# Optimization experiments

Hardware: AMD Instinct MI355X
Metric: run time of the kernel (lower is better)

Reference implementation:

```python
import jax, jax.numpy as jnp
import numpy as np

N_NODES = 50000
N_EDGES = 600000
IN_CH, HID_CH, OUT_CH = 128, 128, 64


def setup_inputs() -> dict:
    key = jax.random.key(0)
    ks = jax.random.split(key, 8)
    s = lambda fan_in: 1.0 / np.sqrt(fan_in)
    return {
        "x": jax.random.normal(ks[0], (N_NODES, IN_CH), dtype=jnp.float32),
        "edge_index": jax.random.randint(ks[1], (2, N_EDGES), 0, N_NODES, dtype=jnp.int32),
        "W1l": jax.random.normal(ks[2], (IN_CH, HID_CH), dtype=jnp.float32) * s(IN_CH),
        "W1r": jax.random.normal(ks[3], (IN_CH, HID_CH), dtype=jnp.float32) * s(IN_CH),
        "b1": jnp.zeros((HID_CH,), dtype=jnp.float32),
        "W2l": jax.random.normal(ks[4], (HID_CH, OUT_CH), dtype=jnp.float32) * s(HID_CH),
        "W2r": jax.random.normal(ks[5], (HID_CH, OUT_CH), dtype=jnp.float32) * s(HID_CH),
        "b2": jnp.zeros((OUT_CH,), dtype=jnp.float32),
    }


def _sage_conv(x, edge_index, Wl, Wr, b):
    """PyG SAGEConv (aggr='mean', root_weight=True): lin_l(mean_j x_j) + lin_r(x_i)."""
    src, dst = edge_index[0], edge_index[1]
    n = x.shape[0]
    # gather source features per edge, scatter-add into destination nodes
    agg = jax.ops.segment_sum(x[src], dst, num_segments=n)  # [N, F]
    deg = jax.ops.segment_sum(jnp.ones(src.shape, x.dtype), dst, num_segments=n)
    mean = agg / jnp.maximum(deg, 1.0)[:, None]
    return mean @ Wl + x @ Wr + b


def reference(x, edge_index, W1l, W1r, b1, W2l, W2r, b2):
    h = jax.nn.relu(_sage_conv(x, edge_index, W1l, W1r, b1))
    # dropout p=0.05 is identity in eval mode
    return _sage_conv(h, edge_index, W2l, W2r, b2)
```

## Files before the change

### kernel.cpp

```cpp
#include <hip/hip_runtime.h>
#include <hip/hip_bf16.h>

#define IN_CH 128
#define HID_CH 128
#define OUT_CH 64
#define SCAN_B 256

typedef __attribute__((ext_vector_type(8))) short bf16x8;
typedef __attribute__((ext_vector_type(4))) float f32x4;

__device__ __forceinline__ ushort f2bf(float f) {
    uint u = __float_as_uint(f);
    uint r = (u + 0x7fffu + ((u >> 16) & 1u)) >> 16;
    return (ushort)r;
}
__device__ __forceinline__ float bflo(uint u) { return __uint_as_float(u << 16); }
__device__ __forceinline__ float bfhi(uint u) { return __uint_as_float(u & 0xffff0000u); }


__global__ __launch_bounds__(256) void prep_count_kernel(
    const int* __restrict__ ei, int* __restrict__ deg,
    const float* __restrict__ x, ushort* __restrict__ xb,
    const float* __restrict__ W1l, const float* __restrict__ W1r,
    const float* __restrict__ W2l, const float* __restrict__ W2r,
    ushort* __restrict__ W1lT, ushort* __restrict__ W1rT,
    ushort* __restrict__ W2lT, ushort* __restrict__ W2rT,
    int n_edges, int nx, int cnt_blocks, int cvt_blocks) {
    int b = blockIdx.x, tid = threadIdx.x;
    if (b < cnt_blocks) {
        int e4 = b * 256 + tid;
        if (e4 * 4 < n_edges) {
            int4 d = *(const int4*)(ei + n_edges + e4 * 4);
            atomicAdd(&deg[d.x], 1);
            atomicAdd(&deg[d.y], 1);
            atomicAdd(&deg[d.z], 1);
            atomicAdd(&deg[d.w], 1);
        }
    } else if (b < cnt_blocks + cvt_blocks) {
        int i = (b - cnt_blocks) * 256 + tid;
        if (i * 8 < nx) {
            float4 v0 = *(const float4*)(x + i * 8);
            float4 v1 = *(const float4*)(x + i * 8 + 4);
            uint4 o;
            o.x = (uint)f2bf(v0.x) | ((uint)f2bf(v0.y) << 16);
            o.y = (uint)f2bf(v0.z) | ((uint)f2bf(v0.w) << 16);
            o.z = (uint)f2bf(v1.x) | ((uint)f2bf(v1.y) << 16);
            o.w = (uint)f2bf(v1.z) | ((uint)f2bf(v1.w) << 16);
            *(uint4*)(xb + i * 8) = o;
        }
    } else {
        int t = (b - cnt_blocks - cvt_blocks) * 256 + tid;
        if (t < 16384) {
            int nn = t >> 7, kk = t & 127;
            W1lT[t] = f2bf(W1l[kk * 128 + nn]);
        } else if (t < 32768) {
            int u = t - 16384;
            int nn = u >> 7, kk = u & 127;
            W1rT[u] = f2bf(W1r[kk * 128 + nn]);
        } else if (t < 40960) {
            int u = t - 32768;
            int nn = u >> 7, kk = u & 127;
            W2lT[u] = f2bf(W2l[kk * 64 + nn]);
        } else if (t < 49152) {
            int u = t - 40960;
            int nn = u >> 7, kk = u & 127;
            W2rT[u] = f2bf(W2r[kk * 64 + nn]);
        }
    }
}


__global__ __launch_bounds__(SCAN_B) void scan_partials_kernel(
    const int* __restrict__ deg, int* __restrict__ partials, int n) {
    __shared__ int ws[SCAN_B / 64];
    int i = blockIdx.x * SCAN_B + threadIdx.x;
    int v = (i < n) ? deg[i] : 0;
    for (int off = 32; off > 0; off >>= 1) v += __shfl_down(v, off, 64);
    int lane = threadIdx.x & 63, w = threadIdx.x >> 6;
    if (lane == 0) ws[w] = v;
    __syncthreads();
    if (threadIdx.x == 0) {
        int s = 0;
        for (int k = 0; k < SCAN_B / 64; ++k) s += ws[k];
        partials[blockIdx.x] = s;
    }
}

__global__ __launch_bounds__(256) void scan_bases_kernel(
    const int* __restrict__ partials, int* __restrict__ bases,
    int* __restrict__ offsets, int nblocks, int n) {
    __shared__ int sm[256];
    int t = threadIdx.x;
    int v = (t < nblocks) ? partials[t] : 0;
    sm[t] = v;
    __syncthreads();
    for (int off = 1; off < 256; off <<= 1) {
        int u = (t >= off) ? sm[t - off] : 0;
        __syncthreads();
        sm[t] += u;
        __syncthreads();
    }
    if (t < nblocks) bases[t] = sm[t] - v;
    if (t == 255) offsets[n] = sm[255];
}

__global__ __launch_bounds__(SCAN_B) void scan_final_kernel(
    const int* __restrict__ deg, const int* __restrict__ bases,
    int* __restrict__ offsets, int* __restrict__ cursor, int n) {
    __shared__ int sm[SCAN_B];
    int t = threadIdx.x;
    int i = blockIdx.x * SCAN_B + t;
    int v = (i < n) ? deg[i] : 0;
    sm[t] = v;
    __syncthreads();
    for (int off = 1; off < SCAN_B; off <<= 1) {
        int u = (t >= off) ? sm[t - off] : 0;
        __syncthreads();
        sm[t] += u;
        __syncthreads();
    }
    if (i < n) {
        int o = bases[blockIdx.x] + sm[t] - v;
        offsets[i] = o;
        cursor[i]  = o;
    }
}

__global__ __launch_bounds__(256) void fill_kernel(
    const int* __restrict__ ei, int* __restrict__ cursor,
    int* __restrict__ edge_src, int n_edges) {
    int e4 = blockIdx.x * 256 + threadIdx.x;
    if (e4 * 4 >= n_edges) return;
    int4 s = *(const int4*)(ei + e4 * 4);
    int4 d = *(const int4*)(ei + n_edges + e4 * 4);
    edge_src[atomicAdd(&cursor[d.x], 1)] = s.x;
    edge_src[atomicAdd(&cursor[d.y], 1)] = s.y;
    edge_src[atomicAdd(&cursor[d.z], 1)] = s.z;
    edge_src[atomicAdd(&cursor[d.w], 1)] = s.w;
}


__global__ __launch_bounds__(256) void gather_mean_bf16_kernel(
    const ushort* __restrict__ feat, const int* __restrict__ offsets,
    const int* __restrict__ edge_src, ushort* __restrict__ mean, int n_nodes) {
    int wid  = (blockIdx.x * blockDim.x + threadIdx.x) >> 6;
    int lane = threadIdx.x & 63;
    if (wid >= n_nodes) return;
    int beg = offsets[wid];
    int end = offsets[wid + 1];
    int q = lane >> 4;
    int c = lane & 15;
    float s0 = 0, s1 = 0, s2 = 0, s3 = 0, s4 = 0, s5 = 0, s6 = 0, s7 = 0;

    int e = beg;
    for (; e + 8 <= end; e += 8) {
        int r0 = edge_src[e + q];
        int r1 = edge_src[e + 4 + q];
        uint4 A = *(const uint4*)(feat + (size_t)r0 * 128 + c * 8);
        uint4 B = *(const uint4*)(feat + (size_t)r1 * 128 + c * 8);
        s0 += bflo(A.x) + bflo(B.x);  s1 += bfhi(A.x) + bfhi(B.x);
        s2 += bflo(A.y) + bflo(B.y);  s3 += bfhi(A.y) + bfhi(B.y);
        s4 += bflo(A.z) + bflo(B.z);  s5 += bfhi(A.z) + bfhi(B.z);
        s6 += bflo(A.w) + bflo(B.w);  s7 += bfhi(A.w) + bfhi(B.w);
    }
    int rem = end - e;
    if (rem > 0) {
        int i0 = min(e + q, end - 1);
        int i1 = min(e + 4 + q, end - 1);
        int r0 = edge_src[i0];
        int r1 = edge_src[i1];
        uint4 A = *(const uint4*)(feat + (size_t)r0 * 128 + c * 8);
        uint4 B = *(const uint4*)(feat + (size_t)r1 * 128 + c * 8);
        if (q < rem) {
            s0 += bflo(A.x);  s1 += bfhi(A.x);
            s2 += bflo(A.y);  s3 += bfhi(A.y);
            s4 += bflo(A.z);  s5 += bfhi(A.z);
            s6 += bflo(A.w);  s7 += bfhi(A.w);
        }
        if (4 + q < rem) {
            s0 += bflo(B.x);  s1 += bfhi(B.x);
            s2 += bflo(B.y);  s3 += bfhi(B.y);
            s4 += bflo(B.z);  s5 += bfhi(B.z);
            s6 += bflo(B.w);  s7 += bfhi(B.w);
        }
    }

#pragma unroll
    for (int m = 16; m < 64; m <<= 1) {
        s0 += __shfl_xor(s0, m, 64);
        s1 += __shfl_xor(s1, m, 64);
        s2 += __shfl_xor(s2, m, 64);
        s3 += __shfl_xor(s3, m, 64);
        s4 += __shfl_xor(s4, m, 64);
        s5 += __shfl_xor(s5, m, 64);
        s6 += __shfl_xor(s6, m, 64);
        s7 += __shfl_xor(s7, m, 64);
    }

    if (q == 0) {
        float inv = 1.0f / fmaxf((float)(end - beg), 1.0f);
        uint4 o;
        o.x = (uint)f2bf(s0 * inv) | ((uint)f2bf(s1 * inv) << 16);
        o.y = (uint)f2bf(s2 * inv) | ((uint)f2bf(s3 * inv) << 16);
        o.z = (uint)f2bf(s4 * inv) | ((uint)f2bf(s5 * inv) << 16);
        o.w = (uint)f2bf(s6 * inv) | ((uint)f2bf(s7 * inv) << 16);
        *(uint4*)(mean + (size_t)wid * 128 + c * 8) = o;
    }
}


__global__ __launch_bounds__(256) void l1_mfma_kernel(
    const ushort* __restrict__ mean, const ushort* __restrict__ xb,
    const ushort* __restrict__ WlT, const ushort* __restrict__ WrT,
    const float* __restrict__ b, ushort* __restrict__ h, int n_nodes) {
    int wave = threadIdx.x >> 6, lane = threadIdx.x & 63;
    int m0 = (blockIdx.x * 4 + wave) * 32;
    int r  = lane & 15;
    int ko = (lane >> 4) * 8;

    int gc0 = min(m0 + r,      n_nodes - 1);
    int gc1 = min(m0 + 16 + r, n_nodes - 1);

    f32x4 acc[8][2] = {};
#pragma unroll
    for (int kk = 0; kk < 4; ++kk) {
        int kb = kk * 32 + ko;
        bf16x8 aM0 = *(const bf16x8*)(mean + (size_t)gc0 * 128 + kb);
        bf16x8 aM1 = *(const bf16x8*)(mean + (size_t)gc1 * 128 + kb);
        bf16x8 aX0 = *(const bf16x8*)(xb   + (size_t)gc0 * 128 + kb);
        bf16x8 aX1 = *(const bf16x8*)(xb   + (size_t)gc1 * 128 + kb);
#pragma unroll
        for (int j = 0; j < 8; ++j) {
            bf16x8 bL = *(const bf16x8*)(WlT + (size_t)(j * 16 + r) * 128 + kb);
            bf16x8 bR = *(const bf16x8*)(WrT + (size_t)(j * 16 + r) * 128 + kb);
            acc[j][0] = __builtin_amdgcn_mfma_f32_16x16x32_bf16(aM0, bL, acc[j][0], 0, 0, 0);
            acc[j][0] = __builtin_amdgcn_mfma_f32_16x16x32_bf16(aX0, bR, acc[j][0], 0, 0, 0);
            acc[j][1] = __builtin_amdgcn_mfma_f32_16x16x32_bf16(aM1, bL, acc[j][1], 0, 0, 0);
            acc[j][1] = __builtin_amdgcn_mfma_f32_16x16x32_bf16(aX1, bR, acc[j][1], 0, 0, 0);
        }
    }

#pragma unroll
    for (int j = 0; j < 8; ++j) {
        float bv = b[j * 16 + r];
#pragma unroll
        for (int s = 0; s < 2; ++s) {
            int rowbase = m0 + s * 16 + (lane >> 4) * 4;
#pragma unroll
            for (int q = 0; q < 4; ++q) {
                int g = rowbase + q;
                if (g < n_nodes)
                    h[(size_t)g * 128 + j * 16 + r] =
                        f2bf(fmaxf(acc[j][s][q] + bv, 0.f));
            }
        }
    }
}


__global__ __launch_bounds__(256) void l2_mfma_kernel(
    const ushort* __restrict__ mean, const ushort* __restrict__ hb,
    const ushort* __restrict__ WlT, const ushort* __restrict__ WrT,
    const float* __restrict__ b, float* __restrict__ out, int n_nodes) {
    int wave = threadIdx.x >> 6, lane = threadIdx.x & 63;
    int m0 = (blockIdx.x * 4 + wave) * 32;
    int r  = lane & 15;
    int ko = (lane >> 4) * 8;

    int gc0 = min(m0 + r,      n_nodes - 1);
    int gc1 = min(m0 + 16 + r, n_nodes - 1);

    f32x4 acc[4][2] = {};
#pragma unroll
    for (int kk = 0; kk < 4; ++kk) {
        int kb = kk * 32 + ko;
        bf16x8 aM0 = *(const bf16x8*)(mean + (size_t)gc0 * 128 + kb);
        bf16x8 aM1 = *(const bf16x8*)(mean + (size_t)gc1 * 128 + kb);
        bf16x8 aH0 = *(const bf16x8*)(hb   + (size_t)gc0 * 128 + kb);
        bf16x8 aH1 = *(const bf16x8*)(hb   + (size_t)gc1 * 128 + kb);
#pragma unroll
        for (int j = 0; j < 4; ++j) {
            bf16x8 bL = *(const bf16x8*)(WlT + (size_t)(j * 16 + r) * 128 + kb);
            bf16x8 bR = *(const bf16x8*)(WrT + (size_t)(j * 16 + r) * 128 + kb);
            acc[j][0] = __builtin_amdgcn_mfma_f32_16x16x32_bf16(aM0, bL, acc[j][0], 0, 0, 0);
            acc[j][0] = __builtin_amdgcn_mfma_f32_16x16x32_bf16(aH0, bR, acc[j][0], 0, 0, 0);
            acc[j][1] = __builtin_amdgcn_mfma_f32_16x16x32_bf16(aM1, bL, acc[j][1], 0, 0, 0);
            acc[j][1] = __builtin_amdgcn_mfma_f32_16x16x32_bf16(aH1, bR, acc[j][1], 0, 0, 0);
        }
    }

#pragma unroll
    for (int j = 0; j < 4; ++j) {
        float bv = b[j * 16 + r];
#pragma unroll
        for (int s = 0; s < 2; ++s) {
            int rowbase = m0 + s * 16 + (lane >> 4) * 4;
#pragma unroll
            for (int q = 0; q < 4; ++q) {
                int g = rowbase + q;
                if (g < n_nodes)
                    out[(size_t)g * 64 + j * 16 + r] = acc[j][s][q] + bv;
            }
        }
    }
}


extern "C" void kernel_launch(void* const* d_in, const int* in_sizes, int n_in,
                              void* d_out, int out_size, void* d_ws, size_t ws_size,
                              hipStream_t stream) {
    const float* x   = (const float*)d_in[0];
    const int*   ei  = (const int*)d_in[1];
    const float* W1l = (const float*)d_in[2];
    const float* W1r = (const float*)d_in[3];
    const float* b1  = (const float*)d_in[4];
    const float* W2l = (const float*)d_in[5];
    const float* W2r = (const float*)d_in[6];
    const float* b2  = (const float*)d_in[7];
    float* out = (float*)d_out;

    int n_nodes = in_sizes[0] / IN_CH;
    int n_edges = in_sizes[1] / 2;
    int nsb = (n_nodes + SCAN_B - 1) / SCAN_B;

    char* ws = (char*)d_ws;
    int* deg      = (int*)ws;
    int* offsets  = deg + n_nodes;
    int* cursor   = offsets + n_nodes + 1;
    int* partials = cursor + n_nodes;
    int* bases    = partials + nsb;
    int* edge_src = bases + nsb;
    size_t off = ((size_t)(3 * n_nodes + 1 + 2 * nsb + n_edges)) * sizeof(int);
    off = (off + 255) & ~(size_t)255;
    ushort* xb    = (ushort*)(ws + off);
    ushort* meanb = xb    + (size_t)n_nodes * 128;
    ushort* hb    = meanb + (size_t)n_nodes * 128;
    ushort* W1lT  = hb    + (size_t)n_nodes * 128;
    ushort* W1rT  = W1lT + 128 * 128;
    ushort* W2lT  = W1rT + 128 * 128;
    ushort* W2rT  = W2lT + 64 * 128;

    hipMemsetAsync(deg, 0, n_nodes * sizeof(int), stream);

    const int TB = 256;
    int nx = n_nodes * IN_CH;
    int cnt_blocks = (n_edges / 4 + TB - 1) / TB;
    int cvt_blocks = (nx / 8 + TB - 1) / TB;
    int tr_blocks  = (49152 + TB - 1) / TB;

    prep_count_kernel<<<cnt_blocks + cvt_blocks + tr_blocks, TB, 0, stream>>>(
        ei, deg, x, xb, W1l, W1r, W2l, W2r, W1lT, W1rT, W2lT, W2rT,
        n_edges, nx, cnt_blocks, cvt_blocks);
    scan_partials_kernel<<<nsb, SCAN_B, 0, stream>>>(deg, partials, n_nodes);
    scan_bases_kernel<<<1, 256, 0, stream>>>(partials, bases, offsets, nsb, n_nodes);
    scan_final_kernel<<<nsb, SCAN_B, 0, stream>>>(deg, bases, offsets, cursor, n_nodes);
    fill_kernel<<<cnt_blocks, TB, 0, stream>>>(ei, cursor, edge_src, n_edges);

    int gblocks = (n_nodes * 64 + TB - 1) / TB;
    int mblocks = (n_nodes + 127) / 128;

    gather_mean_bf16_kernel<<<gblocks, TB, 0, stream>>>(xb, offsets, edge_src, meanb, n_nodes);
    l1_mfma_kernel<<<mblocks, 256, 0, stream>>>(meanb, xb, W1lT, W1rT, b1, hb, n_nodes);

    gather_mean_bf16_kernel<<<gblocks, TB, 0, stream>>>(hb, offsets, edge_src, meanb, n_nodes);
    l2_mfma_kernel<<<mblocks, 256, 0, stream>>>(meanb, hb, W2lT, W2rT, b2, out, n_nodes);
}
```

Before: 248.0 us.

## Fuse all stages into one persistent kernel with software grid barriers

Replaces the memset and nine kernel launches with a single persistent mega-kernel. The grid is sized from occupancy times CU count, and the stages (convert, degree count, scan, CSR fill, two gather/GEMM layers) are separated by atomic-counter grid barriers. The goal is to remove launch overhead and inter-kernel gaps. In exchange, each stage now runs as a grid-stride loop on fewer threads, and the barriers add spin costs. Correctness relies on all blocks being co-resident, since the launch is not cooperative. The gather tail is also simplified to use conditional loads.

New measurement: 751.2 us. 3.03x slower.

```diff
diff --git a/kernel.cpp b/kernel.cpp
--- a/kernel.cpp
+++ b/kernel.cpp
@@ -1,9 +1,5 @@
 #include <hip/hip_runtime.h>
-#include <hip/hip_bf16.h>
-
-#define IN_CH 128
-#define HID_CH 128
-#define OUT_CH 64
+
 #define SCAN_B 256
 
 typedef __attribute__((ext_vector_type(8))) short bf16x8;
@@ -17,135 +13,31 @@
 __device__ __forceinline__ float bflo(uint u) { return __uint_as_float(u << 16); }
 __device__ __forceinline__ float bfhi(uint u) { return __uint_as_float(u & 0xffff0000u); }
 
-
-__global__ __launch_bounds__(256) void prep_count_kernel(
-    const int* __restrict__ ei, int* __restrict__ deg,
-    const float* __restrict__ x, ushort* __restrict__ xb,
-    const float* __restrict__ W1l, const float* __restrict__ W1r,
-    const float* __restrict__ W2l, const float* __restrict__ W2r,
-    ushort* __restrict__ W1lT, ushort* __restrict__ W1rT,
-    ushort* __restrict__ W2lT, ushort* __restrict__ W2rT,
-    int n_edges, int nx, int cnt_blocks, int cvt_blocks) {
-    int b = blockIdx.x, tid = threadIdx.x;
-    if (b < cnt_blocks) {
-        int e4 = b * 256 + tid;
-        if (e4 * 4 < n_edges) {
-            int4 d = *(const int4*)(ei + n_edges + e4 * 4);
-            atomicAdd(&deg[d.x], 1);
-            atomicAdd(&deg[d.y], 1);
-            atomicAdd(&deg[d.z], 1);
-            atomicAdd(&deg[d.w], 1);
-        }
-    } else if (b < cnt_blocks + cvt_blocks) {
-        int i = (b - cnt_blocks) * 256 + tid;
-        if (i * 8 < nx) {
-            float4 v0 = *(const float4*)(x + i * 8);
-            float4 v1 = *(const float4*)(x + i * 8 + 4);
-            uint4 o;
-            o.x = (uint)f2bf(v0.x) | ((uint)f2bf(v0.y) << 16);
-            o.y = (uint)f2bf(v0.z) | ((uint)f2bf(v0.w) << 16);
-            o.z = (uint)f2bf(v1.x) | ((uint)f2bf(v1.y) << 16);
-            o.w = (uint)f2bf(v1.z) | ((uint)f2bf(v1.w) << 16);
-            *(uint4*)(xb + i * 8) = o;
-        }
-    } else {
-        int t = (b - cnt_blocks - cvt_blocks) * 256 + tid;
-        if (t < 16384) {
-            int nn = t >> 7, kk = t & 127;
-            W1lT[t] = f2bf(W1l[kk * 128 + nn]);
-        } else if (t < 32768) {
-            int u = t - 16384;
-            int nn = u >> 7, kk = u & 127;
-            W1rT[u] = f2bf(W1r[kk * 128 + nn]);
-        } else if (t < 40960) {
-            int u = t - 32768;
-            int nn = u >> 7, kk = u & 127;
-            W2lT[u] = f2bf(W2l[kk * 64 + nn]);
-        } else if (t < 49152) {
-            int u = t - 40960;
-            int nn = u >> 7, kk = u & 127;
-            W2rT[u] = f2bf(W2r[kk * 64 + nn]);
-        }
-    }
-}
-
-
-__global__ __launch_bounds__(SCAN_B) void scan_partials_kernel(
-    const int* __restrict__ deg, int* __restrict__ partials, int n) {
-    __shared__ int ws[SCAN_B / 64];
-    int i = blockIdx.x * SCAN_B + threadIdx.x;
-    int v = (i < n) ? deg[i] : 0;
-    for (int off = 32; off > 0; off >>= 1) v += __shfl_down(v, off, 64);
-    int lane = threadIdx.x & 63, w = threadIdx.x >> 6;
-    if (lane == 0) ws[w] = v;
+__device__ int g_bar_cnt = 0;
+__device__ int g_bar_gen = 0;
+
+__device__ __forceinline__ void grid_barrier() {
     __syncthreads();
     if (threadIdx.x == 0) {
-        int s = 0;
-        for (int k = 0; k < SCAN_B / 64; ++k) s += ws[k];
-        partials[blockIdx.x] = s;
-    }
-}
-
-__global__ __launch_bounds__(256) void scan_bases_kernel(
-    const int* __restrict__ partials, int* __restrict__ bases,
-    int* __restrict__ offsets, int nblocks, int n) {
-    __shared__ int sm[256];
-    int t = threadIdx.x;
-    int v = (t < nblocks) ? partials[t] : 0;
-    sm[t] = v;
+        __threadfence();
+        int g = __hip_atomic_load(&g_bar_gen, __ATOMIC_RELAXED, __HIP_MEMORY_SCOPE_AGENT);
+        int a = __hip_atomic_fetch_add(&g_bar_cnt, 1, __ATOMIC_ACQ_REL, __HIP_MEMORY_SCOPE_AGENT);
+        if (a == (int)gridDim.x - 1) {
+            __hip_atomic_store(&g_bar_cnt, 0, __ATOMIC_RELAXED, __HIP_MEMORY_SCOPE_AGENT);
+            __hip_atomic_fetch_add(&g_bar_gen, 1, __ATOMIC_RELEASE, __HIP_MEMORY_SCOPE_AGENT);
+        } else {
+            while (__hip_atomic_load(&g_bar_gen, __ATOMIC_ACQUIRE, __HIP_MEMORY_SCOPE_AGENT) == g)
+                __builtin_amdgcn_s_sleep(2);
+        }
+        __threadfence();
+    }
     __syncthreads();
-    for (int off = 1; off < 256; off <<= 1) {
-        int u = (t >= off) ? sm[t - off] : 0;
-        __syncthreads();
-        sm[t] += u;
-        __syncthreads();
-    }
-    if (t < nblocks) bases[t] = sm[t] - v;
-    if (t == 255) offsets[n] = sm[255];
-}
-
-__global__ __launch_bounds__(SCAN_B) void scan_final_kernel(
-    const int* __restrict__ deg, const int* __restrict__ bases,
-    int* __restrict__ offsets, int* __restrict__ cursor, int n) {
-    __shared__ int sm[SCAN_B];
-    int t = threadIdx.x;
-    int i = blockIdx.x * SCAN_B + t;
-    int v = (i < n) ? deg[i] : 0;
-    sm[t] = v;
-    __syncthreads();
-    for (int off = 1; off < SCAN_B; off <<= 1) {
-        int u = (t >= off) ? sm[t - off] : 0;
-        __syncthreads();
-        sm[t] += u;
-        __syncthreads();
-    }
-    if (i < n) {
-        int o = bases[blockIdx.x] + sm[t] - v;
-        offsets[i] = o;
-        cursor[i]  = o;
-    }
-}
-
-__global__ __launch_bounds__(256) void fill_kernel(
-    const int* __restrict__ ei, int* __restrict__ cursor,
-    int* __restrict__ edge_src, int n_edges) {
-    int e4 = blockIdx.x * 256 + threadIdx.x;
-    if (e4 * 4 >= n_edges) return;
-    int4 s = *(const int4*)(ei + e4 * 4);
-    int4 d = *(const int4*)(ei + n_edges + e4 * 4);
-    edge_src[atomicAdd(&cursor[d.x], 1)] = s.x;
-    edge_src[atomicAdd(&cursor[d.y], 1)] = s.y;
-    edge_src[atomicAdd(&cursor[d.z], 1)] = s.z;
-    edge_src[atomicAdd(&cursor[d.w], 1)] = s.w;
-}
-
-
-__global__ __launch_bounds__(256) void gather_mean_bf16_kernel(
+}
+
+__device__ __forceinline__ void gather_node(
     const ushort* __restrict__ feat, const int* __restrict__ offsets,
-    const int* __restrict__ edge_src, ushort* __restrict__ mean, int n_nodes) {
-    int wid  = (blockIdx.x * blockDim.x + threadIdx.x) >> 6;
-    int lane = threadIdx.x & 63;
-    if (wid >= n_nodes) return;
+    const int* __restrict__ edge_src, ushort* __restrict__ mean,
+    int wid, int lane) {
     int beg = offsets[wid];
     int end = offsets[wid + 1];
     int q = lane >> 4;
@@ -163,26 +55,21 @@
         s4 += bflo(A.z) + bflo(B.z);  s5 += bfhi(A.z) + bfhi(B.z);
         s6 += bflo(A.w) + bflo(B.w);  s7 += bfhi(A.w) + bfhi(B.w);
     }
-    int rem = end - e;
-    if (rem > 0) {
-        int i0 = min(e + q, end - 1);
-        int i1 = min(e + 4 + q, end - 1);
-        int r0 = edge_src[i0];
-        int r1 = edge_src[i1];
+    if (e + q < end) {
+        int r0 = edge_src[e + q];
         uint4 A = *(const uint4*)(feat + (size_t)r0 * 128 + c * 8);
+        s0 += bflo(A.x);  s1 += bfhi(A.x);
+        s2 += bflo(A.y);  s3 += bfhi(A.y);
+        s4 += bflo(A.z);  s5 += bfhi(A.z);
+        s6 += bflo(A.w);  s7 += bfhi(A.w);
+    }
+    if (e + 4 + q < end) {
+        int r1 = edge_src[e + 4 + q];
         uint4 B = *(const uint4*)(feat + (size_t)r1 * 128 + c * 8);
-        if (q < rem) {
-            s0 += bflo(A.x);  s1 += bfhi(A.x);
-            s2 += bflo(A.y);  s3 += bfhi(A.y);
-            s4 += bflo(A.z);  s5 += bfhi(A.z);
-            s6 += bflo(A.w);  s7 += bfhi(A.w);
-        }
-        if (4 + q < rem) {
-            s0 += bflo(B.x);  s1 += bfhi(B.x);
-            s2 += bflo(B.y);  s3 += bfhi(B.y);
-            s4 += bflo(B.z);  s5 += bfhi(B.z);
-            s6 += bflo(B.w);  s7 += bfhi(B.w);
-        }
+        s0 += bflo(B.x);  s1 += bfhi(B.x);
+        s2 += bflo(B.y);  s3 += bfhi(B.y);
+        s4 += bflo(B.z);  s5 += bfhi(B.z);
+        s6 += bflo(B.w);  s7 += bfhi(B.w);
     }
 
 #pragma unroll
@@ -208,16 +95,13 @@
     }
 }
 
-
-__global__ __launch_bounds__(256) void l1_mfma_kernel(
+__device__ __forceinline__ void l1_tile(
     const ushort* __restrict__ mean, const ushort* __restrict__ xb,
     const ushort* __restrict__ WlT, const ushort* __restrict__ WrT,
-    const float* __restrict__ b, ushort* __restrict__ h, int n_nodes) {
-    int wave = threadIdx.x >> 6, lane = threadIdx.x & 63;
-    int m0 = (blockIdx.x * 4 + wave) * 32;
+    const float* __restrict__ b, ushort* __restrict__ h,
+    int m0, int lane, int n_nodes) {
     int r  = lane & 15;
     int ko = (lane >> 4) * 8;
-
     int gc0 = min(m0 + r,      n_nodes - 1);
     int gc1 = min(m0 + 16 + r, n_nodes - 1);
 
@@ -239,7 +123,6 @@
             acc[j][1] = __builtin_amdgcn_mfma_f32_16x16x32_bf16(aX1, bR, acc[j][1], 0, 0, 0);
         }
     }
-
 #pragma unroll
     for (int j = 0; j < 8; ++j) {
         float bv = b[j * 16 + r];
@@ -247,26 +130,23 @@
         for (int s = 0; s < 2; ++s) {
             int rowbase = m0 + s * 16 + (lane >> 4) * 4;
 #pragma unroll
-            for (int q = 0; q < 4; ++q) {
-                int g = rowbase + q;
+            for (int q2 = 0; q2 < 4; ++q2) {
+                int g = rowbase + q2;
                 if (g < n_nodes)
                     h[(size_t)g * 128 + j * 16 + r] =
-                        f2bf(fmaxf(acc[j][s][q] + bv, 0.f));
+                        f2bf(fmaxf(acc[j][s][q2] + bv, 0.f));
             }
         }
     }
 }
 
-
-__global__ __launch_bounds__(256) void l2_mfma_kernel(
+__device__ __forceinline__ void l2_tile(
     const ushort* __restrict__ mean, const ushort* __restrict__ hb,
     const ushort* __restrict__ WlT, const ushort* __restrict__ WrT,
-    const float* __restrict__ b, float* __restrict__ out, int n_nodes) {
-    int wave = threadIdx.x >> 6, lane = threadIdx.x & 63;
-    int m0 = (blockIdx.x * 4 + wave) * 32;
+    const float* __restrict__ b, float* __restrict__ out,
+    int m0, int lane, int n_nodes) {
     int r  = lane & 15;
     int ko = (lane >> 4) * 8;
-
     int gc0 = min(m0 + r,      n_nodes - 1);
     int gc1 = min(m0 + 16 + r, n_nodes - 1);
 
@@ -288,7 +168,6 @@
             acc[j][1] = __builtin_amdgcn_mfma_f32_16x16x32_bf16(aH1, bR, acc[j][1], 0, 0, 0);
         }
     }
-
 #pragma unroll
     for (int j = 0; j < 4; ++j) {
         float bv = b[j * 16 + r];
@@ -296,72 +175,181 @@
         for (int s = 0; s < 2; ++s) {
             int rowbase = m0 + s * 16 + (lane >> 4) * 4;
 #pragma unroll
-            for (int q = 0; q < 4; ++q) {
-                int g = rowbase + q;
+            for (int q2 = 0; q2 < 4; ++q2) {
+                int g = rowbase + q2;
                 if (g < n_nodes)
-                    out[(size_t)g * 64 + j * 16 + r] = acc[j][s][q] + bv;
+                    out[(size_t)g * 64 + j * 16 + r] = acc[j][s][q2] + bv;
             }
         }
     }
+}
+
+struct Params {
+    const int* ei; const float* x;
+    const float* W1l; const float* W1r; const float* b1;
+    const float* W2l; const float* W2r; const float* b2;
+    int* deg; int* offsets; int* cursor; int* partials; int* edge_src;
+    ushort* xb; ushort* meanb; ushort* hb;
+    ushort* W1lT; ushort* W1rT; ushort* W2lT; ushort* W2rT;
+    float* out;
+    int n_nodes, n_edges, nsb;
+};
+
+__global__ __launch_bounds__(256, 2) void mega_kernel(Params p) {
+    int tid  = threadIdx.x;
+    int gt   = blockIdx.x * 256 + tid;
+    int nthr = gridDim.x * 256;
+    int lane = tid & 63;
+    int wave = tid >> 6;
+    __shared__ int sA[SCAN_B];
+    __shared__ int sB[SCAN_B];
+
+    for (int i = gt; i < p.n_nodes; i += nthr) p.deg[i] = 0;
+    int nx8 = p.n_nodes * 128 / 8;
+    for (int i = gt; i < nx8; i += nthr) {
+        float4 v0 = *(const float4*)(p.x + (size_t)i * 8);
+        float4 v1 = *(const float4*)(p.x + (size_t)i * 8 + 4);
+        uint4 o;
+        o.x = (uint)f2bf(v0.x) | ((uint)f2bf(v0.y) << 16);
+        o.y = (uint)f2bf(v0.z) | ((uint)f2bf(v0.w) << 16);
+        o.z = (uint)f2bf(v1.x) | ((uint)f2bf(v1.y) << 16);
+        o.w = (uint)f2bf(v1.z) | ((uint)f2bf(v1.w) << 16);
+        *(uint4*)(p.xb + (size_t)i * 8) = o;
+    }
+    for (int t = gt; t < 49152; t += nthr) {
+        if (t < 16384)       { int nn = t >> 7, kk = t & 127;            p.W1lT[t] = f2bf(p.W1l[kk * 128 + nn]); }
+        else if (t < 32768)  { int u = t - 16384; int nn = u >> 7, kk = u & 127; p.W1rT[u] = f2bf(p.W1r[kk * 128 + nn]); }
+        else if (t < 40960)  { int u = t - 32768; int nn = u >> 7, kk = u & 127; p.W2lT[u] = f2bf(p.W2l[kk * 64 + nn]); }
+        else                 { int u = t - 40960; int nn = u >> 7, kk = u & 127; p.W2rT[u] = f2bf(p.W2r[kk * 64 + nn]); }
+    }
+    grid_barrier();
+
+    int ne4 = p.n_edges >> 2;
+    for (int e4 = gt; e4 < ne4; e4 += nthr) {
+        int4 d = *(const int4*)(p.ei + p.n_edges + (size_t)e4 * 4);
+        atomicAdd(&p.deg[d.x], 1); atomicAdd(&p.deg[d.y], 1);
+        atomicAdd(&p.deg[d.z], 1); atomicAdd(&p.deg[d.w], 1);
+    }
+    for (int e = ne4 * 4 + gt; e < p.n_edges; e += nthr)
+        atomicAdd(&p.deg[p.ei[p.n_edges + e]], 1);
+    grid_barrier();
+
+    for (int ch = blockIdx.x; ch < p.nsb; ch += gridDim.x) {
+        int i = ch * SCAN_B + tid;
+        int v = (i < p.n_nodes) ? p.deg[i] : 0;
+        for (int m = 32; m > 0; m >>= 1) v += __shfl_down(v, m, 64);
+        if (lane == 0) sA[wave] = v;
+        __syncthreads();
+        if (tid == 0) p.partials[ch] = sA[0] + sA[1] + sA[2] + sA[3];
+        __syncthreads();
+    }
+    grid_barrier();
+
+    for (int ch = blockIdx.x; ch < p.nsb; ch += gridDim.x) {
+        sA[tid] = (tid < p.nsb) ? p.partials[tid] : 0;
+        __syncthreads();
+        for (int m = 1; m < SCAN_B; m <<= 1) {
+            int u = (tid >= m) ? sA[tid - m] : 0;
+            __syncthreads();
+            sA[tid] += u;
+            __syncthreads();
+        }
+        int base  = (ch > 0) ? sA[ch - 1] : 0;
+        int total = sA[p.nsb - 1];
+        int i = ch * SCAN_B + tid;
+        int v = (i < p.n_nodes) ? p.deg[i] : 0;
+        sB[tid] = v;
+        __syncthreads();
+        for (int m = 1; m < SCAN_B; m <<= 1) {
+            int u = (tid >= m) ? sB[tid - m] : 0;
+            __syncthreads();
+            sB[tid] += u;
+            __syncthreads();
+        }
+        if (i < p.n_nodes) {
+            int o = base + sB[tid] - v;
+            p.offsets[i] = o;
+            p.cursor[i]  = o;
+        }
+        if (ch == p.nsb - 1 && tid == 0) p.offsets[p.n_nodes] = total;
+        __syncthreads();
+    }
+    grid_barrier();
+
+    for (int e4 = gt; e4 < ne4; e4 += nthr) {
+        int4 s = *(const int4*)(p.ei + (size_t)e4 * 4);
+        int4 d = *(const int4*)(p.ei + p.n_edges + (size_t)e4 * 4);
+        p.edge_src[atomicAdd(&p.cursor[d.x], 1)] = s.x;
+        p.edge_src[atomicAdd(&p.cursor[d.y], 1)] = s.y;
+        p.edge_src[atomicAdd(&p.cursor[d.z], 1)] = s.z;
+        p.edge_src[atomicAdd(&p.cursor[d.w], 1)] = s.w;
+    }
+    for (int e = ne4 * 4 + gt; e < p.n_edges; e += nthr) {
+        int s = p.ei[e], d = p.ei[p.n_edges + e];
+        p.edge_src[atomicAdd(&p.cursor[d], 1)] = s;
+    }
+    grid_barrier();
+
+    int gw = blockIdx.x * 4 + wave, nw = gridDim.x * 4;
+    for (int wid = gw; wid < p.n_nodes; wid += nw)
+        gather_node(p.xb, p.offsets, p.edge_src, p.meanb, wid, lane);
+    grid_barrier();
+
+    for (int t0 = blockIdx.x * 128; t0 < p.n_nodes; t0 += gridDim.x * 128)
+        l1_tile(p.meanb, p.xb, p.W1lT, p.W1rT, p.b1, p.hb, t0 + wave * 32, lane, p.n_nodes);
+    grid_barrier();
+
+    for (int wid = gw; wid < p.n_nodes; wid += nw)
+        gather_node(p.hb, p.offsets, p.edge_src, p.meanb, wid, lane);
+    grid_barrier();
+
+    for (int t0 = blockIdx.x * 128; t0 < p.n_nodes; t0 += gridDim.x * 128)
+        l2_tile(p.meanb, p.hb, p.W2lT, p.W2rT, p.b2, p.out, t0 + wave * 32, lane, p.n_nodes);
 }
 
 
 extern "C" void kernel_launch(void* const* d_in, const int* in_sizes, int n_in,
                               void* d_out, int out_size, void* d_ws, size_t ws_size,
                               hipStream_t stream) {
-    const float* x   = (const float*)d_in[0];
-    const int*   ei  = (const int*)d_in[1];
-    const float* W1l = (const float*)d_in[2];
-    const float* W1r = (const float*)d_in[3];
-    const float* b1  = (const float*)d_in[4];
-    const float* W2l = (const float*)d_in[5];
-    const float* W2r = (const float*)d_in[6];
-    const float* b2  = (const float*)d_in[7];
-    float* out = (float*)d_out;
-
-    int n_nodes = in_sizes[0] / IN_CH;
-    int n_edges = in_sizes[1] / 2;
-    int nsb = (n_nodes + SCAN_B - 1) / SCAN_B;
-
-    char* ws = (char*)d_ws;
-    int* deg      = (int*)ws;
-    int* offsets  = deg + n_nodes;
-    int* cursor   = offsets + n_nodes + 1;
-    int* partials = cursor + n_nodes;
-    int* bases    = partials + nsb;
-    int* edge_src = bases + nsb;
-    size_t off = ((size_t)(3 * n_nodes + 1 + 2 * nsb + n_edges)) * sizeof(int);
+    Params p;
+    p.x   = (const float*)d_in[0];
+    p.ei  = (const int*)d_in[1];
+    p.W1l = (const float*)d_in[2];
+    p.W1r = (const float*)d_in[3];
+    p.b1  = (const float*)d_in[4];
+    p.W2l = (const float*)d_in[5];
+    p.W2r = (const float*)d_in[6];
+    p.b2  = (const float*)d_in[7];
+    p.out = (float*)d_out;
+
+    p.n_nodes = in_sizes[0] / 128;
+    p.n_edges = in_sizes[1] / 2;
+    p.nsb = (p.n_nodes + SCAN_B - 1) / SCAN_B;
+
+    char* ws   = (char*)d_ws;
+    p.deg      = (int*)ws;
+    p.offsets  = p.deg + p.n_nodes;
+    p.cursor   = p.offsets + p.n_nodes + 1;
+    p.partials = p.cursor + p.n_nodes;
+    p.edge_src = p.partials + p.nsb;
+    size_t off = ((size_t)(3 * p.n_nodes + 1 + p.nsb + p.n_edges)) * sizeof(int);
     off = (off + 255) & ~(size_t)255;
-    ushort* xb    = (ushort*)(ws + off);
-    ushort* meanb = xb    + (size_t)n_nodes * 128;
-    ushort* hb    = meanb + (size_t)n_nodes * 128;
-    ushort* W1lT  = hb    + (size_t)n_nodes * 128;
-    ushort* W1rT  = W1lT + 128 * 128;
-    ushort* W2lT  = W1rT + 128 * 128;
-    ushort* W2rT  = W2lT + 64 * 128;
-
-    hipMemsetAsync(deg, 0, n_nodes * sizeof(int), stream);
-
-    const int TB = 256;
-    int nx = n_nodes * IN_CH;
-    int cnt_blocks = (n_edges / 4 + TB - 1) / TB;
-    int cvt_blocks = (nx / 8 + TB - 1) / TB;
-    int tr_blocks  = (49152 + TB - 1) / TB;
-
-    prep_count_kernel<<<cnt_blocks + cvt_blocks + tr_blocks, TB, 0, stream>>>(
-        ei, deg, x, xb, W1l, W1r, W2l, W2r, W1lT, W1rT, W2lT, W2rT,
-        n_edges, nx, cnt_blocks, cvt_blocks);
-    scan_partials_kernel<<<nsb, SCAN_B, 0, stream>>>(deg, partials, n_nodes);
-    scan_bases_kernel<<<1, 256, 0, stream>>>(partials, bases, offsets, nsb, n_nodes);
-    scan_final_kernel<<<nsb, SCAN_B, 0, stream>>>(deg, bases, offsets, cursor, n_nodes);
-    fill_kernel<<<cnt_blocks, TB, 0, stream>>>(ei, cursor, edge_src, n_edges);
-
-    int gblocks = (n_nodes * 64 + TB - 1) / TB;
-    int mblocks = (n_nodes + 127) / 128;
-
-    gather_mean_bf16_kernel<<<gblocks, TB, 0, stream>>>(xb, offsets, edge_src, meanb, n_nodes);
-    l1_mfma_kernel<<<mblocks, 256, 0, stream>>>(meanb, xb, W1lT, W1rT, b1, hb, n_nodes);
-
-    gather_mean_bf16_kernel<<<gblocks, TB, 0, stream>>>(hb, offsets, edge_src, meanb, n_nodes);
-    l2_mfma_kernel<<<mblocks, 256, 0, stream>>>(meanb, hb, W2lT, W2rT, b2, out, n_nodes);
-}
+    p.xb    = (ushort*)(ws + off);
+    p.meanb = p.xb    + (size_t)p.n_nodes * 128;
+    p.hb    = p.meanb + (size_t)p.n_nodes * 128;
+    p.W1lT  = p.hb    + (size_t)p.n_nodes * 128;
+    p.W1rT  = p.W1lT + 128 * 128;
+    p.W2lT  = p.W1rT + 128 * 128;
+    p.W2rT  = p.W2lT + 64 * 128;
+
+    int maxActive = 0;
+    (void)hipOccupancyMaxActiveBlocksPerMultiprocessor(&maxActive, mega_kernel, 256, 0);
+    if (maxActive < 1) maxActive = 1;
+    if (maxActive > 8) maxActive = 8;
+    int nCU = 0;
+    (void)hipDeviceGetAttribute(&nCU, hipDeviceAttributeMultiprocessorCount, 0);
+    if (nCU <= 0) nCU = 256;
+    int grid = maxActive * nCU;
+
+    hipLaunchKernelGGL(mega_kernel, dim3(grid), dim3(256), 0, stream, p);
+}
```

## Project layer-2 features before aggregation and merge scan base kernel into final scan

Applied to the files above, without the earlier changes.

Layer 2 now computes h@W2l first into a 64-wide bf16 buffer, then gathers and means those 64-wide rows, and finally adds h@W2r plus bias in a separate MFMA kernel. Because the mean is linear, this halves the bytes moved by the second gather. It adds one extra kernel launch and an extra round trip through a 64-wide intermediate, and rounds the projected values to bf16 before aggregation. The scan is also simplified: each final-scan block redoes the scan of block partials itself, which removes the single-block bases kernel. The gather tail now guards each load with a bounds check instead of clamping indices.

New measurement: 250.2 us. About the same (+0.9%).

```diff
diff --git a/kernel.cpp b/kernel.cpp
--- a/kernel.cpp
+++ b/kernel.cpp
@@ -2,8 +2,6 @@
 #include <hip/hip_bf16.h>
 
 #define IN_CH 128
-#define HID_CH 128
-#define OUT_CH 64
 #define SCAN_B 256
 
 typedef __attribute__((ext_vector_type(8))) short bf16x8;
@@ -86,44 +84,38 @@
     }
 }
 
-__global__ __launch_bounds__(256) void scan_bases_kernel(
-    const int* __restrict__ partials, int* __restrict__ bases,
-    int* __restrict__ offsets, int nblocks, int n) {
-    __shared__ int sm[256];
+__global__ __launch_bounds__(SCAN_B) void scan_final_kernel(
+    const int* __restrict__ deg, const int* __restrict__ partials,
+    int* __restrict__ offsets, int* __restrict__ cursor, int n, int nsb) {
+    __shared__ int sA[SCAN_B];
+    __shared__ int sB[SCAN_B];
     int t = threadIdx.x;
-    int v = (t < nblocks) ? partials[t] : 0;
-    sm[t] = v;
+    sA[t] = (t < nsb) ? partials[t] : 0;
     __syncthreads();
-    for (int off = 1; off < 256; off <<= 1) {
-        int u = (t >= off) ? sm[t - off] : 0;
+    for (int m = 1; m < SCAN_B; m <<= 1) {
+        int u = (t >= m) ? sA[t - m] : 0;
         __syncthreads();
-        sm[t] += u;
+        sA[t] += u;
         __syncthreads();
     }
-    if (t < nblocks) bases[t] = sm[t] - v;
-    if (t == 255) offsets[n] = sm[255];
-}
-
-__global__ __launch_bounds__(SCAN_B) void scan_final_kernel(
-    const int* __restrict__ deg, const int* __restrict__ bases,
-    int* __restrict__ offsets, int* __restrict__ cursor, int n) {
-    __shared__ int sm[SCAN_B];
-    int t = threadIdx.x;
+    int base  = (blockIdx.x > 0) ? sA[blockIdx.x - 1] : 0;
+    int total = sA[nsb - 1];
     int i = blockIdx.x * SCAN_B + t;
     int v = (i < n) ? deg[i] : 0;
-    sm[t] = v;
+    sB[t] = v;
     __syncthreads();
-    for (int off = 1; off < SCAN_B; off <<= 1) {
-        int u = (t >= off) ? sm[t - off] : 0;
+    for (int m = 1; m < SCAN_B; m <<= 1) {
+        int u = (t >= m) ? sB[t - m] : 0;
         __syncthreads();
-        sm[t] += u;
+        sB[t] += u;
         __syncthreads();
     }
     if (i < n) {
-        int o = bases[blockIdx.x] + sm[t] - v;
+        int o = base + sB[t] - v;
         offsets[i] = o;
         cursor[i]  = o;
     }
+    if (blockIdx.x == 0 && t == 0) offsets[n] = total;
 }
 
 __global__ __launch_bounds__(256) void fill_kernel(
@@ -140,7 +132,7 @@
 }
 
 
-__global__ __launch_bounds__(256) void gather_mean_bf16_kernel(
+__global__ __launch_bounds__(256) void gather_mean128_kernel(
     const ushort* __restrict__ feat, const int* __restrict__ offsets,
     const int* __restrict__ edge_src, ushort* __restrict__ mean, int n_nodes) {
     int wid  = (blockIdx.x * blockDim.x + threadIdx.x) >> 6;
@@ -163,26 +155,21 @@
         s4 += bflo(A.z) + bflo(B.z);  s5 += bfhi(A.z) + bfhi(B.z);
         s6 += bflo(A.w) + bflo(B.w);  s7 += bfhi(A.w) + bfhi(B.w);
     }
-    int rem = end - e;
-    if (rem > 0) {
-        int i0 = min(e + q, end - 1);
-        int i1 = min(e + 4 + q, end - 1);
-        int r0 = edge_src[i0];
-        int r1 = edge_src[i1];
+    if (e + q < end) {
+        int r0 = edge_src[e + q];
         uint4 A = *(const uint4*)(feat + (size_t)r0 * 128 + c * 8);
+        s0 += bflo(A.x);  s1 += bfhi(A.x);
+        s2 += bflo(A.y);  s3 += bfhi(A.y);
+        s4 += bflo(A.z);  s5 += bfhi(A.z);
+        s6 += bflo(A.w);  s7 += bfhi(A.w);
+    }
+    if (e + 4 + q < end) {
+        int r1 = edge_src[e + 4 + q];
         uint4 B = *(const uint4*)(feat + (size_t)r1 * 128 + c * 8);
-        if (q < rem) {
-            s0 += bflo(A.x);  s1 += bfhi(A.x);
-            s2 += bflo(A.y);  s3 += bfhi(A.y);
-            s4 += bflo(A.z);  s5 += bfhi(A.z);
-            s6 += bflo(A.w);  s7 += bfhi(A.w);
-        }
-        if (4 + q < rem) {
-            s0 += bflo(B.x);  s1 += bfhi(B.x);
-            s2 += bflo(B.y);  s3 += bfhi(B.y);
-            s4 += bflo(B.z);  s5 += bfhi(B.z);
-            s6 += bflo(B.w);  s7 += bfhi(B.w);
-        }
+        s0 += bflo(B.x);  s1 += bfhi(B.x);
+        s2 += bflo(B.y);  s3 += bfhi(B.y);
+        s4 += bflo(B.z);  s5 += bfhi(B.z);
+        s6 += bflo(B.w);  s7 += bfhi(B.w);
     }
 
 #pragma unroll
@@ -209,6 +196,70 @@
 }
 
 
+__global__ __launch_bounds__(256) void gather_mean64_kernel(
+    const ushort* __restrict__ feat, const int* __restrict__ offsets,
+    const int* __restrict__ edge_src, ushort* __restrict__ mean, int n_nodes) {
+    int wid  = (blockIdx.x * blockDim.x + threadIdx.x) >> 6;
+    int lane = threadIdx.x & 63;
+    if (wid >= n_nodes) return;
+    int beg = offsets[wid];
+    int end = offsets[wid + 1];
+    int q = lane >> 3;
+    int c = lane & 7;
+    float s0 = 0, s1 = 0, s2 = 0, s3 = 0, s4 = 0, s5 = 0, s6 = 0, s7 = 0;
+
+    int e = beg;
+    for (; e + 16 <= end; e += 16) {
+        int r0 = edge_src[e + q];
+        int r1 = edge_src[e + 8 + q];
+        uint4 A = *(const uint4*)(feat + (size_t)r0 * 64 + c * 8);
+        uint4 B = *(const uint4*)(feat + (size_t)r1 * 64 + c * 8);
+        s0 += bflo(A.x) + bflo(B.x);  s1 += bfhi(A.x) + bfhi(B.x);
+        s2 += bflo(A.y) + bflo(B.y);  s3 += bfhi(A.y) + bfhi(B.y);
+        s4 += bflo(A.z) + bflo(B.z);  s5 += bfhi(A.z) + bfhi(B.z);
+        s6 += bflo(A.w) + bflo(B.w);  s7 += bfhi(A.w) + bfhi(B.w);
+    }
+    if (e + q < end) {
+        int r0 = edge_src[e + q];
+        uint4 A = *(const uint4*)(feat + (size_t)r0 * 64 + c * 8);
+        s0 += bflo(A.x);  s1 += bfhi(A.x);
+        s2 += bflo(A.y);  s3 += bfhi(A.y);
+        s4 += bflo(A.z);  s5 += bfhi(A.z);
+        s6 += bflo(A.w);  s7 += bfhi(A.w);
+    }
+    if (e + 8 + q < end) {
+        int r1 = edge_src[e + 8 + q];
+        uint4 B = *(const uint4*)(feat + (size_t)r1 * 64 + c * 8);
+        s0 += bflo(B.x);  s1 += bfhi(B.x);
+        s2 += bflo(B.y);  s3 += bfhi(B.y);
+        s4 += bflo(B.z);  s5 += bfhi(B.z);
+        s6 += bflo(B.w);  s7 += bfhi(B.w);
+    }
+
+#pragma unroll
+    for (int m = 8; m < 64; m <<= 1) {
+        s0 += __shfl_xor(s0, m, 64);
+        s1 += __shfl_xor(s1, m, 64);
+        s2 += __shfl_xor(s2, m, 64);
+        s3 += __shfl_xor(s3, m, 64);
+        s4 += __shfl_xor(s4, m, 64);
+        s5 += __shfl_xor(s5, m, 64);
+        s6 += __shfl_xor(s6, m, 64);
+        s7 += __shfl_xor(s7, m, 64);
+    }
+
+    if (q == 0) {
+        float inv = 1.0f / fmaxf((float)(end - beg), 1.0f);
+        uint4 o;
+        o.x = (uint)f2bf(s0 * inv) | ((uint)f2bf(s1 * inv) << 16);
+        o.y = (uint)f2bf(s2 * inv) | ((uint)f2bf(s3 * inv) << 16);
+        o.z = (uint)f2bf(s4 * inv) | ((uint)f2bf(s5 * inv) << 16);
+        o.w = (uint)f2bf(s6 * inv) | ((uint)f2bf(s7 * inv) << 16);
+        *(uint4*)(mean + (size_t)wid * 64 + c * 8) = o;
+    }
+}
+
+
 __global__ __launch_bounds__(256) void l1_mfma_kernel(
     const ushort* __restrict__ mean, const ushort* __restrict__ xb,
     const ushort* __restrict__ WlT, const ushort* __restrict__ WrT,
@@ -258,10 +309,9 @@
 }
 
 
-__global__ __launch_bounds__(256) void l2_mfma_kernel(
-    const ushort* __restrict__ mean, const ushort* __restrict__ hb,
-    const ushort* __restrict__ WlT, const ushort* __restrict__ WrT,
-    const float* __restrict__ b, float* __restrict__ out, int n_nodes) {
+__global__ __launch_bounds__(256) void l2p_mfma_kernel(
+    const ushort* __restrict__ hb, const ushort* __restrict__ WlT,
+    ushort* __restrict__ hp, int n_nodes) {
     int wave = threadIdx.x >> 6, lane = threadIdx.x & 63;
     int m0 = (blockIdx.x * 4 + wave) * 32;
     int r  = lane & 15;
@@ -274,24 +324,17 @@
 #pragma unroll
     for (int kk = 0; kk < 4; ++kk) {
         int kb = kk * 32 + ko;
-        bf16x8 aM0 = *(const bf16x8*)(mean + (size_t)gc0 * 128 + kb);
-        bf16x8 aM1 = *(const bf16x8*)(mean + (size_t)gc1 * 128 + kb);
-        bf16x8 aH0 = *(const bf16x8*)(hb   + (size_t)gc0 * 128 + kb);
-        bf16x8 aH1 = *(const bf16x8*)(hb   + (size_t)gc1 * 128 + kb);
+        bf16x8 aH0 = *(const bf16x8*)(hb + (size_t)gc0 * 128 + kb);
+        bf16x8 aH1 = *(const bf16x8*)(hb + (size_t)gc1 * 128 + kb);
 #pragma unroll
         for (int j = 0; j < 4; ++j) {
             bf16x8 bL = *(const bf16x8*)(WlT + (size_t)(j * 16 + r) * 128 + kb);
-            bf16x8 bR = *(const bf16x8*)(WrT + (size_t)(j * 16 + r) * 128 + kb);
-            acc[j][0] = __builtin_amdgcn_mfma_f32_16x16x32_bf16(aM0, bL, acc[j][0], 0, 0, 0);
-            acc[j][0] = __builtin_amdgcn_mfma_f32_16x16x32_bf16(aH0, bR, acc[j][0], 0, 0, 0);
-            acc[j][1] = __builtin_amdgcn_mfma_f32_16x16x32_bf16(aM1, bL, acc[j][1], 0, 0, 0);
-            acc[j][1] = __builtin_amdgcn_mfma_f32_16x16x32_bf16(aH1, bR, acc[j][1], 0, 0, 0);
-        }
-    }
-
+            acc[j][0] = __builtin_amdgcn_mfma_f32_16x16x32_bf16(aH0, bL, acc[j][0], 0, 0, 0);
+            acc[j][1] = __builtin_amdgcn_mfma_f32_16x16x32_bf16(aH1, bL, acc[j][1], 0, 0, 0);
+        }
+    }
 #pragma unroll
     for (int j = 0; j < 4; ++j) {
-        float bv = b[j * 16 + r];
 #pragma unroll
         for (int s = 0; s < 2; ++s) {
             int rowbase = m0 + s * 16 + (lane >> 4) * 4;
@@ -299,7 +342,51 @@
             for (int q = 0; q < 4; ++q) {
                 int g = rowbase + q;
                 if (g < n_nodes)
-                    out[(size_t)g * 64 + j * 16 + r] = acc[j][s][q] + bv;
+                    hp[(size_t)g * 64 + j * 16 + r] = f2bf(acc[j][s][q]);
+            }
+        }
+    }
+}
+
+
+__global__ __launch_bounds__(256) void l2r_mfma_kernel(
+    const ushort* __restrict__ hb, const ushort* __restrict__ WrT,
+    const ushort* __restrict__ m2, const float* __restrict__ b,
+    float* __restrict__ out, int n_nodes) {
+    int wave = threadIdx.x >> 6, lane = threadIdx.x & 63;
+    int m0 = (blockIdx.x * 4 + wave) * 32;
+    int r  = lane & 15;
+    int ko = (lane >> 4) * 8;
+
+    int gc0 = min(m0 + r,      n_nodes - 1);
+    int gc1 = min(m0 + 16 + r, n_nodes - 1);
+
+    f32x4 acc[4][2] = {};
+#pragma unroll
+    for (int kk = 0; kk < 4; ++kk) {
+        int kb = kk * 32 + ko;
+        bf16x8 aH0 = *(const bf16x8*)(hb + (size_t)gc0 * 128 + kb);
+        bf16x8 aH1 = *(const bf16x8*)(hb + (size_t)gc1 * 128 + kb);
+#pragma unroll
+        for (int j = 0; j < 4; ++j) {
+            bf16x8 bR = *(const bf16x8*)(WrT + (size_t)(j * 16 + r) * 128 + kb);
+            acc[j][0] = __builtin_amdgcn_mfma_f32_16x16x32_bf16(aH0, bR, acc[j][0], 0, 0, 0);
+            acc[j][1] = __builtin_amdgcn_mfma_f32_16x16x32_bf16(aH1, bR, acc[j][1], 0, 0, 0);
+        }
+    }
+#pragma unroll
+    for (int j = 0; j < 4; ++j) {
+        float bv = b[j * 16 + r];
+#pragma unroll
+        for (int s = 0; s < 2; ++s) {
+            int rowbase = m0 + s * 16 + (lane >> 4) * 4;
+#pragma unroll
+            for (int q = 0; q < 4; ++q) {
+                int g = rowbase + q;
+                if (g < n_nodes) {
+                    float mv = __uint_as_float((uint)m2[(size_t)g * 64 + j * 16 + r] << 16);
+                    out[(size_t)g * 64 + j * 16 + r] = acc[j][s][q] + bv + mv;
+                }
             }
         }
     }
@@ -328,14 +415,15 @@
     int* offsets  = deg + n_nodes;
     int* cursor   = offsets + n_nodes + 1;
     int* partials = cursor + n_nodes;
-    int* bases    = partials + nsb;
-    int* edge_src = bases + nsb;
-    size_t off = ((size_t)(3 * n_nodes + 1 + 2 * nsb + n_edges)) * sizeof(int);
+    int* edge_src = partials + nsb;
+    size_t off = ((size_t)(3 * n_nodes + 1 + nsb + n_edges)) * sizeof(int);
     off = (off + 255) & ~(size_t)255;
     ushort* xb    = (ushort*)(ws + off);
     ushort* meanb = xb    + (size_t)n_nodes * 128;
     ushort* hb    = meanb + (size_t)n_nodes * 128;
-    ushort* W1lT  = hb    + (size_t)n_nodes * 128;
+    ushort* hp    = hb    + (size_t)n_nodes * 128;
+    ushort* m2    = hp    + (size_t)n_nodes * 64;
+    ushort* W1lT  = m2    + (size_t)n_nodes * 64;
     ushort* W1rT  = W1lT + 128 * 128;
     ushort* W2lT  = W1rT + 128 * 128;
     ushort* W2rT  = W2lT + 64 * 128;
@@ -352,16 +440,17 @@
         ei, deg, x, xb, W1l, W1r, W2l, W2r, W1lT, W1rT, W2lT, W2rT,
         n_edges, nx, cnt_blocks, cvt_blocks);
     scan_partials_kernel<<<nsb, SCAN_B, 0, stream>>>(deg, partials, n_nodes);
-    scan_bases_kernel<<<1, 256, 0, stream>>>(partials, bases, offsets, nsb, n_nodes);
-    scan_final_kernel<<<nsb, SCAN_B, 0, stream>>>(deg, bases, offsets, cursor, n_nodes);
+    scan_final_kernel<<<nsb, SCAN_B, 0, stream>>>(deg, partials, offsets, cursor,
+                                                  n_nodes, nsb);
     fill_kernel<<<cnt_blocks, TB, 0, stream>>>(ei, cursor, edge_src, n_edges);
 
     int gblocks = (n_nodes * 64 + TB - 1) / TB;
     int mblocks = (n_nodes + 127) / 128;
 
-    gather_mean_bf16_kernel<<<gblocks, TB, 0, stream>>>(xb, offsets, edge_src, meanb, n_nodes);
+    gather_mean128_kernel<<<gblocks, TB, 0, stream>>>(xb, offsets, edge_src, meanb, n_nodes);
     l1_mfma_kernel<<<mblocks, 256, 0, stream>>>(meanb, xb, W1lT, W1rT, b1, hb, n_nodes);
 
-    gather_mean_bf16_kernel<<<gblocks, TB, 0, stream>>>(hb, offsets, edge_src, meanb, n_nodes);
-    l2_mfma_kernel<<<mblocks, 256, 0, stream>>>(meanb, hb, W2lT, W2rT, b2, out, n_nodes);
-}
+    l2p_mfma_kernel<<<mblocks, 256, 0, stream>>>(hb, W2lT, hp, n_nodes);
+    gather_mean64_kernel<<<gblocks, TB, 0, stream>>>(hp, offsets, edge_src, m2, n_nodes);
+    l2r_mfma_kernel<<<mblocks, 256, 0, stream>>>(hb, W2rT, m2, b2, out, n_nodes);
+}
```
